# Kernel tuning notes

Measured on AMD Instinct MI355X. Metric: run time of the kernel, lower is better.

## Reference

```python
import jax, jax.numpy as jnp
import numpy as np

EPS = 1e-5

def _act_quant(x):
    # per-token int8 absmax quantization with STE passthrough
    s = 127.0 / jnp.clip(jnp.max(jnp.abs(x), axis=-1, keepdims=True), EPS, None)
    xq = jnp.clip(jnp.round(x * s), -128.0, 127.0) / s
    return x + jax.lax.stop_gradient(xq - x)

def _weight_quant(w):
    # ternary {-1,0,1} abs-mean quantization with STE passthrough
    s = 1.0 / jnp.clip(jnp.mean(jnp.abs(w)), EPS, None)
    wq = jnp.clip(jnp.round(w * s), -1.0, 1.0) / s
    return w + jax.lax.stop_gradient(wq - w)

def bitlinear(x, w, b=None):
    y = _act_quant(x) @ _weight_quant(w).T
    return y if b is None else y + b

def setup_inputs() -> dict:
    key = jax.random.key(0)
    ks = jax.random.split(key, 6)
    B, T, C = 64, 256, 1024
    std = 1.0 / np.sqrt(C)
    return {
        "x": jax.random.normal(ks[0], (B, T, C), dtype=jnp.float32),
        "Wq": jax.random.normal(ks[1], (C, C), dtype=jnp.float32) * std,
        "Wk": jax.random.normal(ks[2], (C, C), dtype=jnp.float32) * std,
        "Wv": jax.random.normal(ks[3], (C, C), dtype=jnp.float32) * std,
        "Wp": jax.random.normal(ks[4], (C, C), dtype=jnp.float32) * std,
        "bp": jnp.zeros((C,), dtype=jnp.float32),
        "n_head": 16,
    }

def reference(x, Wq, Wk, Wv, Wp, bp, n_head):
    B, T, C = x.shape
    hd = C // n_head
    def heads(t):  # [B,T,C] -> [B,H,T,hd]
        return t.reshape(B, T, n_head, hd).transpose(0, 2, 1, 3)
    q = heads(bitlinear(x, Wq))
    k = heads(bitlinear(x, Wk))
    v = heads(bitlinear(x, Wv))
    attn = jnp.einsum("bhqd,bhkd->bhqk", q, k) * (1.0 / np.sqrt(hd))
    causal = jnp.tril(jnp.ones((T, T), dtype=bool))
    attn = jnp.where(causal, attn, -jnp.inf)
    attn = jax.nn.softmax(attn, axis=-1)
    y = jnp.einsum("bhqk,bhkd->bhqd", attn, v)
    y = y.transpose(0, 2, 1, 3).reshape(B, T, C)
    return bitlinear(y, Wp, bp)
```

## Files before the change

### kernel.cpp

```cpp
#include <hip/hip_runtime.h>
#include <math.h>

#define AS1 __attribute__((address_space(1)))
#define AS3 __attribute__((address_space(3)))

typedef unsigned short u16;
typedef signed char i8;
typedef short bf16x8 __attribute__((ext_vector_type(8)));
typedef float f32x4 __attribute__((ext_vector_type(4)));
typedef int i32x4 __attribute__((ext_vector_type(4)));

static constexpr int BB = 64, T = 256, C = 1024, H = 16, HD = 64;
static constexpr int M = BB * T;
static constexpr float EPSF = 1e-5f;

static constexpr size_t W8_OFF   = 0;
static constexpr size_t XQ8_OFF  = 4ull  << 20;
static constexpr size_t RSX_OFF  = 20ull << 20;
static constexpr size_t RSY_OFF  = (20ull << 20) + (64 << 10);
static constexpr size_t WSUM_OFF = (20ull << 20) + (128 << 10);
static constexpr size_t WPART_OFF= WSUM_OFF + 64;
static constexpr size_t QB_OFF   = 21ull << 20;
static constexpr size_t KB_OFF   = 53ull << 20;
static constexpr size_t VT_OFF   = 85ull << 20;

__device__ __forceinline__ u16 f2bf_rne(float f) {
    unsigned x = __float_as_uint(f);
    unsigned r = x + 0x7FFF + ((x >> 16) & 1);
    return (u16)(r >> 16);
}

__global__ __launch_bounds__(256) void wsum1_kernel(const float* __restrict__ Wq,
    const float* __restrict__ Wk, const float* __restrict__ Wv,
    const float* __restrict__ Wp, double* __restrict__ wpart)
{
    const int mat = blockIdx.x >> 6;
    const float* W = (mat == 0) ? Wq : (mat == 1) ? Wk : (mat == 2) ? Wv : Wp;
    const int t = threadIdx.x;
    const int base = (blockIdx.x & 63) * 256 + t;
    double s = 0.0;
    for (int i = 0; i < 64; ++i) s += (double)fabsf(W[base + (i << 14)]);
    #pragma unroll
    for (int off = 32; off >= 1; off >>= 1) s += __shfl_down(s, off);
    __shared__ double red[4];
    if ((t & 63) == 0) red[t >> 6] = s;
    __syncthreads();
    if (t == 0) wpart[blockIdx.x] = red[0] + red[1] + red[2] + red[3];
}

__global__ __launch_bounds__(256) void wsum2_kernel(const double* __restrict__ wpart,
                                                    double* __restrict__ wsum)
{
    const int t = threadIdx.x;
    double s = wpart[t];
    #pragma unroll
    for (int off = 32; off >= 1; off >>= 1) s += __shfl_down(s, off);
    if ((t & 63) == 0) wsum[t >> 6] = s;
}

__global__ __launch_bounds__(256) void wquant_kernel(const float* __restrict__ Wq,
    const float* __restrict__ Wk, const float* __restrict__ Wv,
    const float* __restrict__ Wp, const double* __restrict__ wsum,
    i8* __restrict__ w8)
{
    const int mat = blockIdx.x >> 10;
    const float* W = (mat == 0) ? Wq : (mat == 1) ? Wk : (mat == 2) ? Wv : Wp;
    const float mean = (float)(wsum[mat] * (1.0 / 1048576.0));
    const float s = 1.0f / fmaxf(mean, EPSF);
    const int idx = (blockIdx.x & 1023) * 256 + threadIdx.x;
    float4 w = ((const float4*)W)[idx];
    char4 o;
    o.x = (i8)(int)fminf(fmaxf(rintf(w.x * s), -1.f), 1.f);
    o.y = (i8)(int)fminf(fmaxf(rintf(w.y * s), -1.f), 1.f);
    o.z = (i8)(int)fminf(fmaxf(rintf(w.z * s), -1.f), 1.f);
    o.w = (i8)(int)fminf(fmaxf(rintf(w.w * s), -1.f), 1.f);
    ((char4*)(w8 + (size_t)mat * 1048576))[idx] = o;
}

__global__ __launch_bounds__(256) void actquant_kernel(const float* __restrict__ x,
    i8* __restrict__ xq, float* __restrict__ rs)
{
    const int row = blockIdx.x;
    const int t = threadIdx.x;
    float4 v = ((const float4*)(x + (size_t)row * C))[t];
    float m = fmaxf(fmaxf(fabsf(v.x), fabsf(v.y)), fmaxf(fabsf(v.z), fabsf(v.w)));
    #pragma unroll
    for (int off = 32; off >= 1; off >>= 1) m = fmaxf(m, __shfl_down(m, off));
    __shared__ float red[4];
    if ((t & 63) == 0) red[t >> 6] = m;
    __syncthreads();
    float mm = fmaxf(fmaxf(red[0], red[1]), fmaxf(red[2], red[3]));
    mm = fmaxf(mm, EPSF);
    const float s = 127.0f / mm;
    if (t == 0) rs[row] = mm / 127.0f;
    char4 o;
    o.x = (i8)(int)fminf(fmaxf(rintf(v.x * s), -128.f), 127.f);
    o.y = (i8)(int)fminf(fmaxf(rintf(v.y * s), -128.f), 127.f);
    o.z = (i8)(int)fminf(fmaxf(rintf(v.z * s), -128.f), 127.f);
    o.w = (i8)(int)fminf(fmaxf(rintf(v.w * s), -128.f), 127.f);
    ((char4*)(xq + (size_t)row * C))[t] = o;
}

template<bool QKV, int NNB>
__global__ __launch_bounds__(512, 2) void gemm_kernel(const i8* __restrict__ A,
    const i8* __restrict__ w8, const float* __restrict__ rs_row,
    const double* __restrict__ wsum, u16* __restrict__ qb, u16* __restrict__ kb,
    u16* __restrict__ vt, float* __restrict__ outp, const float* __restrict__ bias)
{
    constexpr int K = 1024, N = 1024;
    constexpr int NT = 16;
    __shared__ __align__(16) i8 Asm[4][256 * 64];
    __shared__ __align__(16) i8 Bsm[4][256 * 64];

    const int t = threadIdx.x;

    const int nwg = NNB * 64;
    const int wg = (int)blockIdx.x;
    const int swz = (wg & 7) * (nwg >> 3) + (wg >> 3);
    const int mb = swz / NNB, nb = swz % NNB;
    const int m0 = mb * 256;
    const int mat = QKV ? (nb >> 2) : 3;
    const int n0m = QKV ? ((nb & 3) * 256) : (nb * 256);
    const i8* Bw = w8 + (size_t)mat * 1048576;

    const int lane = t & 63, wv = t >> 6;
    const int wm = wv >> 2, wn = wv & 3;
    const int mr = lane & 15, quad = lane >> 4;

    const int g1 = t, g2 = t + 512;
    const int L1 = (g1 * 16) ^ (((g1 >> 3) & 7) << 4);
    const int L2 = (g2 * 16) ^ (((g2 >> 3) & 7) << 4);
    const i8* a1 = A  + (size_t)(m0  + (L1 >> 6)) * K + (L1 & 63);
    const i8* a2 = A  + (size_t)(m0  + (L2 >> 6)) * K + (L2 & 63);
    const i8* b1 = Bw + (size_t)(n0m + (L1 >> 6)) * K + (L1 & 63);
    const i8* b2 = Bw + (size_t)(n0m + (L2 >> 6)) * K + (L2 & 63);

    const int vvs = (mr >> 1) & 7;
    int aoff[8], boff[4];
    #pragma unroll
    for (int m = 0; m < 8; ++m)
        aoff[m] = ((wm * 128 + m * 16 + mr) * 64 + quad * 16) ^ (vvs << 4);
    #pragma unroll
    for (int n = 0; n < 4; ++n)
        boff[n] = ((wn * 64 + n * 16 + mr) * 64 + quad * 16) ^ (vvs << 4);

    i32x4 acc[8][4];
    #pragma unroll
    for (int m = 0; m < 8; ++m)
        #pragma unroll
        for (int n = 0; n < 4; ++n) acc[m][n] = (i32x4){0, 0, 0, 0};

    #pragma unroll
    for (int p = 0; p < 2; ++p) {
        const int k0 = p * 64;
        __builtin_amdgcn_global_load_lds((const AS1 void*)(a1 + k0), (AS3 void*)&Asm[p][g1 * 16], 16, 0, 0);
        __builtin_amdgcn_global_load_lds((const AS1 void*)(a2 + k0), (AS3 void*)&Asm[p][g2 * 16], 16, 0, 0);
        __builtin_amdgcn_global_load_lds((const AS1 void*)(b1 + k0), (AS3 void*)&Bsm[p][g1 * 16], 16, 0, 0);
        __builtin_amdgcn_global_load_lds((const AS1 void*)(b2 + k0), (AS3 void*)&Bsm[p][g2 * 16], 16, 0, 0);
    }
    asm volatile("s_waitcnt vmcnt(4)" ::: "memory");
    __builtin_amdgcn_s_barrier();
    __builtin_amdgcn_sched_barrier(0);

    for (int tt = 0; tt < NT; ++tt) {
        const i8* Ac = Asm[tt & 3];
        const i8* Bc = Bsm[tt & 3];
        i8* An = Asm[(tt + 2) & 3];
        i8* Bn = Bsm[(tt + 2) & 3];
        const int kn = (tt + 2) * 64;

        if (tt < NT - 2) {
            __builtin_amdgcn_global_load_lds((const AS1 void*)(a1 + kn), (AS3 void*)&An[g1 * 16], 16, 0, 0);
            __builtin_amdgcn_global_load_lds((const AS1 void*)(a2 + kn), (AS3 void*)&An[g2 * 16], 16, 0, 0);
            __builtin_amdgcn_global_load_lds((const AS1 void*)(b1 + kn), (AS3 void*)&Bn[g1 * 16], 16, 0, 0);
            __builtin_amdgcn_global_load_lds((const AS1 void*)(b2 + kn), (AS3 void*)&Bn[g2 * 16], 16, 0, 0);
        }

        i32x4 af[8], bf[4];
        #pragma unroll
        for (int m = 0; m < 8; ++m) af[m] = *(const i32x4*)&Ac[aoff[m]];
        #pragma unroll
        for (int n = 0; n < 4; ++n) bf[n] = *(const i32x4*)&Bc[boff[n]];

        __builtin_amdgcn_s_setprio(1);
        #pragma unroll
        for (int m = 0; m < 8; ++m)
            #pragma unroll
            for (int n = 0; n < 4; ++n)
                acc[m][n] = __builtin_amdgcn_mfma_i32_16x16x64_i8(af[m], bf[n], acc[m][n], 0, 0, 0);
        __builtin_amdgcn_s_setprio(0);

        if (tt < NT - 2) {
            asm volatile("s_waitcnt vmcnt(4)" ::: "memory");
        } else if (tt < NT - 1) {
            asm volatile("s_waitcnt vmcnt(0)" ::: "memory");
        }
        __builtin_amdgcn_s_barrier();
        __builtin_amdgcn_sched_barrier(0);
    }

    float wsc = fmaxf((float)(wsum[mat] * (1.0 / 1048576.0)), EPSF);
    if (QKV && mat == 0) wsc *= 0.125f;

    if (QKV && mat == 2) {
        #pragma unroll
        for (int m = 0; m < 8; ++m) {
            const int gr0 = m0 + wm * 128 + m * 16 + quad * 4;
            const int bbi = gr0 >> 8, tl = gr0 & 255;
            const float4 rs4 = *(const float4*)(rs_row + gr0);
            #pragma unroll
            for (int n = 0; n < 4; ++n) {
                const int gcol = n0m + wn * 64 + n * 16 + mr;
                ushort4 o;
                o.x = f2bf_rne((float)acc[m][n][0] * rs4.x * wsc);
                o.y = f2bf_rne((float)acc[m][n][1] * rs4.y * wsc);
                o.z = f2bf_rne((float)acc[m][n][2] * rs4.z * wsc);
                o.w = f2bf_rne((float)acc[m][n][3] * rs4.w * wsc);
                *(ushort4*)(vt + (size_t)(bbi * 1024 + gcol) * 256 + tl) = o;
            }
        }
        return;
    }

    u16* ob = QKV ? ((mat == 0) ? qb : kb) : nullptr;
    #pragma unroll
    for (int m = 0; m < 8; ++m) {
        const int gr0 = m0 + wm * 128 + m * 16 + quad * 4;
        #pragma unroll
        for (int r = 0; r < 4; ++r) {
            const int grow = gr0 + r;
            const float sc = rs_row[grow] * wsc;
            #pragma unroll
            for (int n = 0; n < 4; ++n) {
                const int gcol = n0m + wn * 64 + n * 16 + mr;
                const float val = (float)acc[m][n][r] * sc;
                if (QKV) {
                    ob[(size_t)grow * N + gcol] = f2bf_rne(val);
                } else {
                    outp[(size_t)grow * N + gcol] = val + bias[gcol];
                }
            }
        }
    }
}

__global__ __launch_bounds__(256) void attn_kernel(const u16* __restrict__ qb,
    const u16* __restrict__ kb, const u16* __restrict__ vt, float* __restrict__ y)
{
    const int t = threadIdx.x;
    const int i = (int)blockIdx.x;
    const int qt = 3 - ((i >> 3) & 3);
    const int bh = ((i >> 5) << 3) | (i & 7);
    const int b = bh >> 4, h = bh & 15;
    const int w = t >> 6, lane = t & 63;
    const int cl = lane & 15, quad = lane >> 4;
    const size_t gb = (size_t)(b * T) * 1024 + h * 64;
    const u16* vtb = vt + (size_t)(b * 1024 + h * 64) * 256;

    const int qrow = qt * 64 + w * 16;
    const int jtiles = (qrow >> 4) + 1;

    const u16* qrp = qb + gb + (size_t)(qrow + cl) * 1024 + quad * 8;
    bf16x8 qf0 = *(const bf16x8*)qrp;
    bf16x8 qf1 = *(const bf16x8*)(qrp + 32);

    f32x4 Sp[16];
    #pragma unroll
    for (int i2 = 0; i2 < 16; ++i2) Sp[i2] = (f32x4){0.f, 0.f, 0.f, 0.f};

    const u16* krp = kb + gb + (size_t)cl * 1024 + quad * 8;
    #pragma unroll
    for (int jt = 0; jt < 16; ++jt) {
        if (jt < jtiles) {
            const u16* kp = krp + (size_t)(jt * 16) * 1024;
            bf16x8 kf0 = *(const bf16x8*)kp;
            bf16x8 kf1 = *(const bf16x8*)(kp + 32);
            Sp[jt] = __builtin_amdgcn_mfma_f32_16x16x32_bf16(kf0, qf0, Sp[jt], 0, 0, 0);
            Sp[jt] = __builtin_amdgcn_mfma_f32_16x16x32_bf16(kf1, qf1, Sp[jt], 0, 0, 0);
            if (jt == jtiles - 1) {
                #pragma unroll
                for (int r = 0; r < 4; ++r)
                    if (quad * 4 + r > cl) Sp[jt][r] = -INFINITY;
            }
        }
    }

    float mx = -INFINITY;
    #pragma unroll
    for (int jt = 0; jt < 16; ++jt) if (jt < jtiles) {
        #pragma unroll
        for (int r = 0; r < 4; ++r) mx = fmaxf(mx, Sp[jt][r]);
    }
    mx = fmaxf(mx, __shfl_xor(mx, 16));
    mx = fmaxf(mx, __shfl_xor(mx, 32));
    float l = 0.f;
    #pragma unroll
    for (int jt = 0; jt < 16; ++jt) if (jt < jtiles) {
        #pragma unroll
        for (int r = 0; r < 4; ++r) {
            float p = __expf(Sp[jt][r] - mx);
            Sp[jt][r] = p;
            l += p;
        }
    }
    l += __shfl_xor(l, 16);
    l += __shfl_xor(l, 32);

    f32x4 O[4];
    #pragma unroll
    for (int i2 = 0; i2 < 4; ++i2) O[i2] = (f32x4){0.f, 0.f, 0.f, 0.f};

    const int s01 = ((quad & 1) << 5) + cl;
    const bool lo = quad < 2;
    #pragma unroll
    for (int jc = 0; jc < 8; ++jc) {
        if (jc * 2 < jtiles) {
            int pk[2][2];
            #pragma unroll
            for (int s = 0; s < 2; ++s) {
                const f32x4 v = Sp[jc * 2 + s];
                pk[s][0] = (int)((unsigned)f2bf_rne(v[0]) | ((unsigned)f2bf_rne(v[1]) << 16));
                pk[s][1] = (int)((unsigned)f2bf_rne(v[2]) | ((unsigned)f2bf_rne(v[3]) << 16));
            }
            int a0 = __shfl(pk[0][0], s01),      a1 = __shfl(pk[0][1], s01);
            int a2 = __shfl(pk[0][0], s01 + 16), a3 = __shfl(pk[0][1], s01 + 16);
            int b0 = __shfl(pk[1][0], s01),      b1 = __shfl(pk[1][1], s01);
            int b2 = __shfl(pk[1][0], s01 + 16), b3 = __shfl(pk[1][1], s01 + 16);
            union { int i[4]; bf16x8 v; } af;
            af.i[0] = lo ? a0 : b0;
            af.i[1] = lo ? a1 : b1;
            af.i[2] = lo ? a2 : b2;
            af.i[3] = lo ? a3 : b3;
            const u16* vp = vtb + (size_t)cl * 256 + jc * 32 + quad * 8;
            #pragma unroll
            for (int dt = 0; dt < 4; ++dt) {
                bf16x8 vf = *(const bf16x8*)(vp + (size_t)dt * 16 * 256);
                O[dt] = __builtin_amdgcn_mfma_f32_16x16x32_bf16(af.v, vf, O[dt], 0, 0, 0);
            }
        }
    }

    float inv[4];
    #pragma unroll
    for (int r = 0; r < 4; ++r) inv[r] = 1.0f / __shfl(l, quad * 4 + r);
    #pragma unroll
    for (int dt = 0; dt < 4; ++dt)
        #pragma unroll
        for (int r = 0; r < 4; ++r)
            y[gb + (size_t)(qrow + quad * 4 + r) * 1024 + dt * 16 + cl] = O[dt][r] * inv[r];
}

extern "C" void kernel_launch(void* const* d_in, const int* in_sizes, int n_in,
                              void* d_out, int out_size, void* d_ws, size_t ws_size,
                              hipStream_t stream) {
    (void)in_sizes; (void)n_in; (void)out_size; (void)ws_size;
    const float* x  = (const float*)d_in[0];
    const float* Wq = (const float*)d_in[1];
    const float* Wk = (const float*)d_in[2];
    const float* Wv = (const float*)d_in[3];
    const float* Wp = (const float*)d_in[4];
    const float* bp = (const float*)d_in[5];
    float* out = (float*)d_out;
    char* ws = (char*)d_ws;

    i8*     w8   = (i8*)(ws + W8_OFF);
    i8*     xq8  = (i8*)(ws + XQ8_OFF);
    float*  rsx  = (float*)(ws + RSX_OFF);
    float*  rsy  = (float*)(ws + RSY_OFF);
    double* wsum = (double*)(ws + WSUM_OFF);
    double* wpart= (double*)(ws + WPART_OFF);
    u16*    qb   = (u16*)(ws + QB_OFF);
    u16*    kb   = (u16*)(ws + KB_OFF);
    u16*    vt   = (u16*)(ws + VT_OFF);

    wsum1_kernel<<<256, 256, 0, stream>>>(Wq, Wk, Wv, Wp, wpart);
    wsum2_kernel<<<1, 256, 0, stream>>>(wpart, wsum);
    wquant_kernel<<<4096, 256, 0, stream>>>(Wq, Wk, Wv, Wp, wsum, w8);
    actquant_kernel<<<M, 256, 0, stream>>>(x, xq8, rsx);

    gemm_kernel<true, 12><<<768, 512, 0, stream>>>(xq8, w8, rsx, wsum, qb, kb, vt, nullptr, nullptr);

    attn_kernel<<<4 * 1024, 256, 0, stream>>>(qb, kb, vt, out);

    actquant_kernel<<<M, 256, 0, stream>>>(out, xq8, rsy);
    gemm_kernel<false, 4><<<256, 512, 0, stream>>>(xq8, w8, rsy, wsum, nullptr, nullptr, nullptr, out, bp);
}
```

Baseline: 350.2 us.

## Pre-pack ternary weights in MFMA fragment order and load B directly to registers

The weight quantization kernel now writes int8 weights in a packed layout matching the MFMA B-fragment order, so each lane reads its 16-byte fragment with one contiguous global load. The GEMM drops the B shared-memory buffers and their async LDS copies, reading B straight from global (L2-resident) memory each k-step. This halves LDS use and LDS traffic per iteration but puts global-load latency directly in front of the MFMAs, with no explicit prefetch. The attention kernel's block-to-(batch,head,q-tile) mapping is also changed to a simpler ordering.

```diff
diff --git a/kernel.cpp b/kernel.cpp
--- a/kernel.cpp
+++ b/kernel.cpp
@@ -63,18 +63,20 @@
     const float* __restrict__ Wp, const double* __restrict__ wsum,
     i8* __restrict__ w8)
 {
-    const int mat = blockIdx.x >> 10;
+    const int mat = blockIdx.x >> 8;
     const float* W = (mat == 0) ? Wq : (mat == 1) ? Wk : (mat == 2) ? Wv : Wp;
     const float mean = (float)(wsum[mat] * (1.0 / 1048576.0));
     const float s = 1.0f / fmaxf(mean, EPSF);
-    const int idx = (blockIdx.x & 1023) * 256 + threadIdx.x;
-    float4 w = ((const float4*)W)[idx];
-    char4 o;
-    o.x = (i8)(int)fminf(fmaxf(rintf(w.x * s), -1.f), 1.f);
-    o.y = (i8)(int)fminf(fmaxf(rintf(w.y * s), -1.f), 1.f);
-    o.z = (i8)(int)fminf(fmaxf(rintf(w.z * s), -1.f), 1.f);
-    o.w = (i8)(int)fminf(fmaxf(rintf(w.w * s), -1.f), 1.f);
-    ((char4*)(w8 + (size_t)mat * 1048576))[idx] = o;
+    const int g = (blockIdx.x & 255) * 256 + threadIdx.x;
+    const int lane = g & 63, kt = (g >> 6) & 15, nt = g >> 10;
+    const int row = nt * 16 + (lane & 15);
+    const int k0 = kt * 64 + (lane >> 4) * 16;
+    const float* src = W + (size_t)row * 1024 + k0;
+    union { i8 b[16]; i32x4 v; } o;
+    #pragma unroll
+    for (int j = 0; j < 16; ++j)
+        o.b[j] = (i8)(int)fminf(fmaxf(rintf(src[j] * s), -1.f), 1.f);
+    *(i32x4*)(w8 + ((size_t)mat << 20) + (size_t)g * 16) = o.v;
 }
 
 __global__ __launch_bounds__(256) void actquant_kernel(const float* __restrict__ x,
@@ -110,7 +112,6 @@
     constexpr int K = 1024, N = 1024;
     constexpr int NT = 16;
     __shared__ __align__(16) i8 Asm[4][256 * 64];
-    __shared__ __align__(16) i8 Bsm[4][256 * 64];
 
     const int t = threadIdx.x;
 
@@ -121,7 +122,7 @@
     const int m0 = mb * 256;
     const int mat = QKV ? (nb >> 2) : 3;
     const int n0m = QKV ? ((nb & 3) * 256) : (nb * 256);
-    const i8* Bw = w8 + (size_t)mat * 1048576;
+    const i8* Bw = w8 + ((size_t)mat << 20);
 
     const int lane = t & 63, wv = t >> 6;
     const int wm = wv >> 2, wn = wv & 3;
@@ -130,19 +131,17 @@
     const int g1 = t, g2 = t + 512;
     const int L1 = (g1 * 16) ^ (((g1 >> 3) & 7) << 4);
     const int L2 = (g2 * 16) ^ (((g2 >> 3) & 7) << 4);
-    const i8* a1 = A  + (size_t)(m0  + (L1 >> 6)) * K + (L1 & 63);
-    const i8* a2 = A  + (size_t)(m0  + (L2 >> 6)) * K + (L2 & 63);
-    const i8* b1 = Bw + (size_t)(n0m + (L1 >> 6)) * K + (L1 & 63);
-    const i8* b2 = Bw + (size_t)(n0m + (L2 >> 6)) * K + (L2 & 63);
+    const i8* a1 = A + (size_t)(m0 + (L1 >> 6)) * K + (L1 & 63);
+    const i8* a2 = A + (size_t)(m0 + (L2 >> 6)) * K + (L2 & 63);
 
     const int vvs = (mr >> 1) & 7;
-    int aoff[8], boff[4];
+    int aoff[8];
     #pragma unroll
     for (int m = 0; m < 8; ++m)
         aoff[m] = ((wm * 128 + m * 16 + mr) * 64 + quad * 16) ^ (vvs << 4);
-    #pragma unroll
-    for (int n = 0; n < 4; ++n)
-        boff[n] = ((wn * 64 + n * 16 + mr) * 64 + quad * 16) ^ (vvs << 4);
+
+    const int ntb = (n0m >> 4) + wn * 4;
+    const i8* bfp = Bw + (size_t)ntb * 16384 + (size_t)lane * 16;
 
     i32x4 acc[8][4];
     #pragma unroll
@@ -155,32 +154,29 @@
         const int k0 = p * 64;
         __builtin_amdgcn_global_load_lds((const AS1 void*)(a1 + k0), (AS3 void*)&Asm[p][g1 * 16], 16, 0, 0);
         __builtin_amdgcn_global_load_lds((const AS1 void*)(a2 + k0), (AS3 void*)&Asm[p][g2 * 16], 16, 0, 0);
-        __builtin_amdgcn_global_load_lds((const AS1 void*)(b1 + k0), (AS3 void*)&Bsm[p][g1 * 16], 16, 0, 0);
-        __builtin_amdgcn_global_load_lds((const AS1 void*)(b2 + k0), (AS3 void*)&Bsm[p][g2 * 16], 16, 0, 0);
-    }
-    asm volatile("s_waitcnt vmcnt(4)" ::: "memory");
+    }
+    asm volatile("s_waitcnt vmcnt(2)" ::: "memory");
     __builtin_amdgcn_s_barrier();
     __builtin_amdgcn_sched_barrier(0);
 
     for (int tt = 0; tt < NT; ++tt) {
         const i8* Ac = Asm[tt & 3];
-        const i8* Bc = Bsm[tt & 3];
         i8* An = Asm[(tt + 2) & 3];
-        i8* Bn = Bsm[(tt + 2) & 3];
         const int kn = (tt + 2) * 64;
+
+        i32x4 bf[4];
+        #pragma unroll
+        for (int n = 0; n < 4; ++n)
+            bf[n] = *(const i32x4*)(bfp + (size_t)n * 16384 + tt * 1024);
 
         if (tt < NT - 2) {
             __builtin_amdgcn_global_load_lds((const AS1 void*)(a1 + kn), (AS3 void*)&An[g1 * 16], 16, 0, 0);
             __builtin_amdgcn_global_load_lds((const AS1 void*)(a2 + kn), (AS3 void*)&An[g2 * 16], 16, 0, 0);
-            __builtin_amdgcn_global_load_lds((const AS1 void*)(b1 + kn), (AS3 void*)&Bn[g1 * 16], 16, 0, 0);
-            __builtin_amdgcn_global_load_lds((const AS1 void*)(b2 + kn), (AS3 void*)&Bn[g2 * 16], 16, 0, 0);
-        }
-
-        i32x4 af[8], bf[4];
+        }
+
+        i32x4 af[8];
         #pragma unroll
         for (int m = 0; m < 8; ++m) af[m] = *(const i32x4*)&Ac[aoff[m]];
-        #pragma unroll
-        for (int n = 0; n < 4; ++n) bf[n] = *(const i32x4*)&Bc[boff[n]];
 
         __builtin_amdgcn_s_setprio(1);
         #pragma unroll
@@ -191,7 +187,7 @@
         __builtin_amdgcn_s_setprio(0);
 
         if (tt < NT - 2) {
-            asm volatile("s_waitcnt vmcnt(4)" ::: "memory");
+            asm volatile("s_waitcnt vmcnt(2)" ::: "memory");
         } else if (tt < NT - 1) {
             asm volatile("s_waitcnt vmcnt(0)" ::: "memory");
         }
@@ -248,9 +244,8 @@
     const u16* __restrict__ kb, const u16* __restrict__ vt, float* __restrict__ y)
 {
     const int t = threadIdx.x;
-    const int i = (int)blockIdx.x;
-    const int qt = 3 - ((i >> 3) & 3);
-    const int bh = ((i >> 5) << 3) | (i & 7);
+    const int qt = 3 - (int)(blockIdx.x >> 10);
+    const int bh = blockIdx.x & 1023;
     const int b = bh >> 4, h = bh & 15;
     const int w = t >> 6, lane = t & 63;
     const int cl = lane & 15, quad = lane >> 4;
@@ -375,7 +370,7 @@
 
     wsum1_kernel<<<256, 256, 0, stream>>>(Wq, Wk, Wv, Wp, wpart);
     wsum2_kernel<<<1, 256, 0, stream>>>(wpart, wsum);
-    wquant_kernel<<<4096, 256, 0, stream>>>(Wq, Wk, Wv, Wp, wsum, w8);
+    wquant_kernel<<<1024, 256, 0, stream>>>(Wq, Wk, Wv, Wp, wsum, w8);
     actquant_kernel<<<M, 256, 0, stream>>>(x, xq8, rsx);
 
     gemm_kernel<true, 12><<<768, 512, 0, stream>>>(xq8, w8, rsx, wsum, qb, kb, vt, nullptr, nullptr);
```

New measurement: 319.0 us. -8.9%, faster.
